# Performance work log

Hardware: AMD Instinct MI355X
Metric: run time of the kernel (lower is better)

Reference implementation:

```python
import jax, jax.numpy as jnp
import numpy as np

B = 4
T, Hh, Ww = 16, 32, 32
C = 256
HEADS = 8
WIN = 4
SHIFT = 2
MLP = 1024


def _rel_pos_index(w):
    coords = np.stack(np.meshgrid(np.arange(w), np.arange(w), np.arange(w), indexing='ij')).reshape(3, -1)
    rc = (coords[:, :, None] - coords[:, None, :]).transpose(1, 2, 0)
    rc[:, :, 0] += w - 1
    rc[:, :, 1] += w - 1
    rc[:, :, 2] += w - 1
    rc[:, :, 0] *= (2 * w - 1) * (2 * w - 1)
    rc[:, :, 1] *= 2 * w - 1
    return rc.sum(-1).astype(np.int32)  # (w^3, w^3)


def _attn_mask(t, h, w, win, shift):
    m = np.zeros((t, h, w))
    sl = (slice(0, -win), slice(-win, -shift), slice(-shift, None))
    cnt = 0
    for a in sl:
        for b in sl:
            for c in sl:
                m[a, b, c] = cnt
                cnt += 1
    m = m.reshape(t // win, win, h // win, win, w // win, win).transpose(0, 2, 4, 1, 3, 5).reshape(-1, win ** 3)
    am = m[:, None, :] - m[:, :, None]  # (nW, N, N)
    return np.where(am != 0, -100.0, 0.0).astype(np.float32)


def setup_inputs() -> dict:
    key = jax.random.key(0)
    ks = jax.random.split(key, 12)
    s_in = 1.0 / np.sqrt(C)
    s_mlp = 1.0 / np.sqrt(MLP)
    return {
        'x': jax.random.normal(ks[0], (B, T * Hh * Ww, C), jnp.float32),
        'norm1_g': jnp.ones((C,), jnp.float32),
        'norm1_b': jnp.zeros((C,), jnp.float32),
        'qkv_w': jax.random.normal(ks[1], (C, 3 * C), jnp.float32) * s_in,
        'qkv_b': jax.random.normal(ks[2], (3 * C,), jnp.float32) * 0.02,
        'proj_w': jax.random.normal(ks[3], (C, C), jnp.float32) * s_in,
        'proj_b': jax.random.normal(ks[4], (C,), jnp.float32) * 0.02,
        'rel_bias_table': jax.random.normal(ks[5], ((2 * WIN - 1) ** 3, HEADS), jnp.float32) * 0.02,
        'norm2_g': jnp.ones((C,), jnp.float32),
        'norm2_b': jnp.zeros((C,), jnp.float32),
        'mlp_w1': jax.random.normal(ks[6], (C, MLP), jnp.float32) * s_in,
        'mlp_b1': jax.random.normal(ks[7], (MLP,), jnp.float32) * 0.02,
        'mlp_w2': jax.random.normal(ks[8], (MLP, C), jnp.float32) * s_mlp,
        'mlp_b2': jax.random.normal(ks[9], (C,), jnp.float32) * 0.02,
        'rel_index': jnp.asarray(_rel_pos_index(WIN)),
        'attn_mask': jnp.asarray(_attn_mask(T, Hh, Ww, WIN, SHIFT)),
    }


def _ln(x, g, b, eps):
    mu = x.mean(-1, keepdims=True)
    var = ((x - mu) ** 2).mean(-1, keepdims=True)
    return (x - mu) * jax.lax.rsqrt(var + eps) * g + b


def reference(x, norm1_g, norm1_b, qkv_w, qkv_b, proj_w, proj_b, rel_bias_table,
              norm2_g, norm2_b, mlp_w1, mlp_b1, mlp_w2, mlp_b2, rel_index, attn_mask):
    w = WIN
    N = w ** 3
    hd = C // HEADS
    scale = hd ** -0.5

    h = _ln(x, norm1_g, norm1_b, 1e-5).reshape(B, T, Hh, Ww, C)
    h = jnp.roll(h, shift=(-SHIFT, -SHIFT, -SHIFT), axis=(1, 2, 3))
    # window partition -> (B*nW, N, C)
    h = h.reshape(B, T // w, w, Hh // w, w, Ww // w, w, C)
    h = h.transpose(0, 1, 3, 5, 2, 4, 6, 7).reshape(-1, N, C)

    qkv = (h @ qkv_w + qkv_b).reshape(-1, N, 3, HEADS, hd)
    qkv = qkv.transpose(2, 0, 3, 1, 4)  # (3, BW, heads, N, hd)
    q, k, v = qkv[0] * scale, qkv[1], qkv[2]
    attn = jnp.einsum('bhid,bhjd->bhij', q, k)

    bias = rel_bias_table[rel_index.reshape(-1)].reshape(N, N, HEADS).transpose(2, 0, 1)
    attn = attn + bias[None]

    nW = attn_mask.shape[0]
    attn = attn.reshape(-1, nW, HEADS, N, N) + attn_mask[None, :, None]
    attn = jax.nn.softmax(attn.reshape(-1, HEADS, N, N), axis=-1)

    o = jnp.einsum('bhij,bhjd->bhid', attn, v).transpose(0, 2, 1, 3).reshape(-1, N, C)
    o = o @ proj_w + proj_b
    # window reverse
    o = o.reshape(B, T // w, Hh // w, Ww // w, w, w, w, C)
    o = o.transpose(0, 1, 4, 2, 5, 3, 6, 7).reshape(B, T, Hh, Ww, C)
    o = jnp.roll(o, shift=(SHIFT, SHIFT, SHIFT), axis=(1, 2, 3)).reshape(B, T * Hh * Ww, C)

    x = x + o
    y = _ln(x, norm2_g, norm2_b, 1e-6)
    y = jax.nn.gelu(y @ mlp_w1 + mlp_b1, approximate=False) @ mlp_w2 + mlp_b2
    return x + y
```

## Files before the change

kernel.cpp:

```cpp
#include <hip/hip_runtime.h>
#include <cstdint>
#include <cstddef>

typedef float  f32x4_t  __attribute__((ext_vector_type(4)));
typedef __bf16 bf16x8_t __attribute__((ext_vector_type(8)));
typedef __bf16 bf16x4_t __attribute__((ext_vector_type(4)));

#define NTOK   65536
#define CCH    256
#define NWINT  1024

__device__ __forceinline__ float wred_sum(float v) {
#pragma unroll
  for (int off = 32; off > 0; off >>= 1) v += __shfl_xor(v, off, 64);
  return v;
}

__device__ __forceinline__ void gload16(void* lds, const void* g) {
  __builtin_amdgcn_global_load_lds(
      (const __attribute__((address_space(1))) uint32_t*)g,
      (__attribute__((address_space(3))) uint32_t*)lds, 16, 0, 0);
}

__device__ __forceinline__ int win_to_orig(int token) {
  int gid = token >> 6, n = token & 63;
  int bb = gid >> 8, rem = gid & 255;
  int t = (((rem >> 6) << 2) + (n >> 4) + 2) & 15;
  int h = ((((rem >> 3) & 7) << 2) + ((n >> 2) & 3) + 2) & 31;
  int w = (((rem & 7) << 2) + (n & 3) + 2) & 31;
  return ((bb * 16 + t) * 32 + h) * 32 + w;
}

__global__ __launch_bounds__(256) void prep_weights(
    const float* __restrict__ qkv_w, const float* __restrict__ proj_w,
    const float* __restrict__ mlp_w1, const float* __restrict__ mlp_w2,
    __bf16* __restrict__ wt_qkv, __bf16* __restrict__ wt_proj,
    __bf16* __restrict__ wt_mlp1, __bf16* __restrict__ wt_mlp2) {
  int i = blockIdx.x * 256 + threadIdx.x;
  if (i < 196608) {
    int k = i / 768, n = i % 768;
    wt_qkv[n * 256 + k] = (__bf16)qkv_w[i];
  } else if (i < 262144) {
    int j = i - 196608;
    int k = j >> 8, n = j & 255;
    wt_proj[n * 256 + k] = (__bf16)proj_w[j];
  } else if (i < 524288) {
    int j = i - 262144;
    int k = j >> 10, n = j & 1023;
    wt_mlp1[n * 256 + k] = (__bf16)mlp_w1[j];
  } else {
    int j = i - 524288;
    int k = j >> 8, n = j & 255;
    wt_mlp2[n * 1024 + k] = (__bf16)mlp_w2[j];
  }
}

__global__ __launch_bounds__(256) void cm_prep(
    const float* __restrict__ table, const int* __restrict__ ridx,
    const float* __restrict__ mask, __bf16* __restrict__ cm) {
  int tid = blockIdx.x * 256 + threadIdx.x;
  int l = tid & 63;
  int t16 = (tid >> 6) & 15;
  int h = (tid >> 10) & 7;
  int w = tid >> 13;
  int it = t16 & 3, jt = t16 >> 2;
  int i = it * 16 + (l & 15);
  int jb = jt * 16 + ((l >> 4) << 2);
  const float* mrow = mask + (size_t)w * 4096 + i * 64;
  const int* rrow = ridx + i * 64;
  bf16x4_t o;
#pragma unroll
  for (int r = 0; r < 4; ++r) {
    int j = jb + r;
    o[r] = (__bf16)(table[rrow[j] * 8 + h] + mrow[j]);
  }
  *(bf16x4_t*)(cm + (size_t)tid * 4) = o;
}

template <int MODE>
__global__ __launch_bounds__(256) void ln_kernel(
    const float* __restrict__ xin, const float* __restrict__ g,
    const float* __restrict__ b, __bf16* __restrict__ out, float eps) {
  int token = blockIdx.x * 4 + (threadIdx.x >> 6);
  int lane = threadIdx.x & 63;
  size_t src = (MODE == 0) ? (size_t)win_to_orig(token) : (size_t)token;
  f32x4_t v = ((const f32x4_t*)(xin + src * CCH))[lane];
  float mu = wred_sum(v[0] + v[1] + v[2] + v[3]) * (1.0f / 256.0f);
  float d0 = v[0] - mu, d1 = v[1] - mu, d2 = v[2] - mu, d3 = v[3] - mu;
  float var = wred_sum(d0 * d0 + d1 * d1 + d2 * d2 + d3 * d3) * (1.0f / 256.0f);
  float rs = rsqrtf(var + eps);
  f32x4_t gg = ((const f32x4_t*)g)[lane];
  f32x4_t bb = ((const f32x4_t*)b)[lane];
  bf16x4_t o;
  o[0] = (__bf16)(d0 * rs * gg[0] + bb[0]);
  o[1] = (__bf16)(d1 * rs * gg[1] + bb[1]);
  o[2] = (__bf16)(d2 * rs * gg[2] + bb[2]);
  o[3] = (__bf16)(d3 * rs * gg[3] + bb[3]);
  *(bf16x4_t*)(out + (size_t)token * CCH + lane * 4) = o;
}

#define BMG 128
#define BNG 256
#define BKG 64
template <int EPI>
__global__ __launch_bounds__(512, 4) void gemm_kernel(
    const __bf16* __restrict__ A, const __bf16* __restrict__ Bt,
    const float* __restrict__ bias, const float* __restrict__ res,
    void* __restrict__ outp, int M, int N, int K) {
  __shared__ __bf16 smA[BMG * BKG];
  __shared__ __bf16 smB[BNG * BKG];
  const int wv = threadIdx.x >> 6;
  const int ln = threadIdx.x & 63;
  const int i15 = ln & 15, g = ln >> 4;

  int nwg = gridDim.x;
  int wgid = ((int)blockIdx.x & 7) * (nwg >> 3) + ((int)blockIdx.x >> 3);
  int nx = N >> 8;
  int bx = wgid % nx, by = wgid / nx;
  const int bm = by * BMG, bn = bx * BNG;
  const int wr = wv >> 2, wc = wv & 3;

  const __bf16* aP[2];
  const __bf16* bP[4];
#pragma unroll
  for (int it = 0; it < 2; ++it) {
    int slot = (it * 8 + wv) * 64 + ln;
    int row = slot >> 3;
    int chunk = (slot & 7) ^ (row & 7);
    aP[it] = A + (size_t)(bm + row) * K + chunk * 8;
  }
#pragma unroll
  for (int it = 0; it < 4; ++it) {
    int slot = (it * 8 + wv) * 64 + ln;
    int row = slot >> 3;
    int chunk = (slot & 7) ^ (row & 7);
    bP[it] = Bt + (size_t)(bn + row) * K + chunk * 8;
  }

  f32x4_t acc[4][4];
#pragma unroll
  for (int m = 0; m < 4; ++m)
#pragma unroll
    for (int n = 0; n < 4; ++n) acc[m][n] = (f32x4_t){0.f, 0.f, 0.f, 0.f};

  const int KT = K >> 6;
  for (int kt = 0; kt < KT; ++kt) {
#pragma unroll
    for (int it = 0; it < 2; ++it) {
      gload16(&smA[(it * 8 + wv) * 512], aP[it]);
      aP[it] += BKG;
    }
#pragma unroll
    for (int it = 0; it < 4; ++it) {
      gload16(&smB[(it * 8 + wv) * 512], bP[it]);
      bP[it] += BKG;
    }
    asm volatile("s_waitcnt vmcnt(0)" ::: "memory");
    __syncthreads();

#pragma unroll
    for (int kh = 0; kh < 2; ++kh) {
      int co = ((kh * 4 + g) ^ (i15 & 7)) * 8;
      bf16x8_t af[4], bfr[4];
#pragma unroll
      for (int m = 0; m < 4; ++m)
        af[m] = *(const bf16x8_t*)(smA + (wr * 64 + m * 16 + i15) * 64 + co);
#pragma unroll
      for (int n = 0; n < 4; ++n)
        bfr[n] = *(const bf16x8_t*)(smB + (wc * 64 + n * 16 + i15) * 64 + co);
#pragma unroll
      for (int m = 0; m < 4; ++m)
#pragma unroll
        for (int n = 0; n < 4; ++n)
          acc[m][n] = __builtin_amdgcn_mfma_f32_16x16x32_bf16(
              af[m], bfr[n], acc[m][n], 0, 0, 0);
    }
    __syncthreads();
  }

  float bv[4];
#pragma unroll
  for (int n = 0; n < 4; ++n) bv[n] = bias[bn + wc * 64 + n * 16 + i15];
#pragma unroll
  for (int m = 0; m < 4; ++m) {
    int grow0 = bm + wr * 64 + m * 16 + g * 4;
#pragma unroll
    for (int r = 0; r < 4; ++r) {
      int grow = grow0 + r;
      size_t rowbase;
      if constexpr (EPI == 1)
        rowbase = (size_t)win_to_orig(grow) * CCH;
      else
        rowbase = (size_t)grow * N;
#pragma unroll
      for (int n = 0; n < 4; ++n) {
        int gcol = bn + wc * 64 + n * 16 + i15;
        float v = acc[m][n][r] + bv[n];
        if constexpr (EPI == 0) {
          ((__bf16*)outp)[rowbase + gcol] = (__bf16)v;
        } else if constexpr (EPI == 1) {
          size_t dst = rowbase + gcol;
          ((float*)outp)[dst] = res[dst] + v;
        } else if constexpr (EPI == 2) {
          float u = v * (0.7978845608028654f + 0.03567740814f * v * v);
          float t = 1.0f - 2.0f / (__expf(2.0f * u) + 1.0f);
          float gl = 0.5f * v * (1.0f + t);
          ((__bf16*)outp)[rowbase + gcol] = (__bf16)gl;
        } else {
          size_t o = rowbase + gcol;
          ((float*)outp)[o] = res[o] + v;
        }
      }
    }
  }
}

__global__ __launch_bounds__(256) void attn_mfma(
    const __bf16* __restrict__ qkv, const __bf16* __restrict__ cm,
    __bf16* __restrict__ owin) {
  __shared__ __align__(16) __bf16 smP[4][64 * 72];
  __shared__ __align__(16) __bf16 smV[4][64 * 32];
  const int wv = threadIdx.x >> 6;
  const int ln = threadIdx.x & 63;
  const int task = blockIdx.x * 4 + wv;
  const int win = task >> 3;
  const int h = task & 7;
  const int i15 = ln & 15, g = ln >> 4;

  const __bf16* base = qkv + (size_t)win * 64 * 768 + h * 32;

  {
    __bf16* vdst = smV[wv];
#pragma unroll
    for (int c = 0; c < 4; ++c) {
      const __bf16* src =
          base + (size_t)(c * 16 + (ln >> 2)) * 768 + 512 + (ln & 3) * 8;
      gload16(vdst + c * 512, src);
    }
  }

  bf16x8_t kf[4], qf[4];
#pragma unroll
  for (int t = 0; t < 4; ++t) {
    kf[t] = *(const bf16x8_t*)(base + (size_t)(t * 16 + i15) * 768 + 256 + g * 8);
    qf[t] = *(const bf16x8_t*)(base + (size_t)(t * 16 + i15) * 768 + g * 8);
  }

  f32x4_t st[4][4];
#pragma unroll
  for (int jt = 0; jt < 4; ++jt)
#pragma unroll
    for (int it = 0; it < 4; ++it)
      st[jt][it] = __builtin_amdgcn_mfma_f32_16x16x32_bf16(
          kf[jt], qf[it], (f32x4_t){0.f, 0.f, 0.f, 0.f}, 0, 0, 0);

  const __bf16* cmp = cm + (((size_t)(win & 255) * 8 + h) * 16) * 256;
#pragma unroll
  for (int jt = 0; jt < 4; ++jt)
#pragma unroll
    for (int it = 0; it < 4; ++it) {
      bf16x4_t c4 = *(const bf16x4_t*)(cmp + ((jt * 4 + it) * 64 + ln) * 4);
#pragma unroll
      for (int r = 0; r < 4; ++r)
        st[jt][it][r] =
            fmaf(st[jt][it][r], 0.17677669529663687f, (float)c4[r]);
    }

#pragma unroll
  for (int it = 0; it < 4; ++it) {
    float mx = -1e30f;
#pragma unroll
    for (int jt = 0; jt < 4; ++jt)
#pragma unroll
      for (int r = 0; r < 4; ++r) mx = fmaxf(mx, st[jt][it][r]);
    mx = fmaxf(mx, __shfl_xor(mx, 16, 64));
    mx = fmaxf(mx, __shfl_xor(mx, 32, 64));
    float sum = 0.f;
#pragma unroll
    for (int jt = 0; jt < 4; ++jt)
#pragma unroll
      for (int r = 0; r < 4; ++r) {
        float p = __expf(st[jt][it][r] - mx);
        st[jt][it][r] = p;
        sum += p;
      }
    sum += __shfl_xor(sum, 16, 64);
    sum += __shfl_xor(sum, 32, 64);
    float inv = 1.0f / sum;
#pragma unroll
    for (int jt = 0; jt < 4; ++jt) {
      bf16x4_t p4;
#pragma unroll
      for (int r = 0; r < 4; ++r) p4[r] = (__bf16)(st[jt][it][r] * inv);
      *(bf16x4_t*)(smP[wv] + (it * 16 + i15) * 72 + jt * 16 + g * 4) = p4;
    }
  }
  __syncthreads();

  f32x4_t oacc[4][2];
#pragma unroll
  for (int it = 0; it < 4; ++it)
#pragma unroll
    for (int dt = 0; dt < 2; ++dt) oacc[it][dt] = (f32x4_t){0.f, 0.f, 0.f, 0.f};

  const __bf16* pl = smP[wv];
  const __bf16* vl = smV[wv];
#pragma unroll
  for (int kt = 0; kt < 2; ++kt) {
    bf16x8_t vf[2];
#pragma unroll
    for (int dt = 0; dt < 2; ++dt)
#pragma unroll
      for (int e = 0; e < 8; ++e)
        vf[dt][e] = vl[(kt * 32 + g * 8 + e) * 32 + dt * 16 + i15];
#pragma unroll
    for (int it = 0; it < 4; ++it) {
      bf16x8_t pa =
          *(const bf16x8_t*)(pl + (it * 16 + i15) * 72 + kt * 32 + g * 8);
#pragma unroll
      for (int dt = 0; dt < 2; ++dt)
        oacc[it][dt] = __builtin_amdgcn_mfma_f32_16x16x32_bf16(
            pa, vf[dt], oacc[it][dt], 0, 0, 0);
    }
  }

  __bf16* op = owin + (size_t)win * 64 * 256 + h * 32;
#pragma unroll
  for (int it = 0; it < 4; ++it)
#pragma unroll
    for (int r = 0; r < 4; ++r) {
      int i = it * 16 + g * 4 + r;
#pragma unroll
      for (int dt = 0; dt < 2; ++dt)
        op[(size_t)i * 256 + dt * 16 + i15] = (__bf16)oacc[it][dt][r];
    }
}

extern "C" void kernel_launch(void* const* d_in, const int* in_sizes, int n_in,
                              void* d_out, int out_size, void* d_ws,
                              size_t ws_size, hipStream_t stream) {
  (void)in_sizes; (void)n_in; (void)out_size; (void)ws_size;
  const float* x      = (const float*)d_in[0];
  const float* n1g    = (const float*)d_in[1];
  const float* n1b    = (const float*)d_in[2];
  const float* qkv_w  = (const float*)d_in[3];
  const float* qkv_b  = (const float*)d_in[4];
  const float* proj_w = (const float*)d_in[5];
  const float* proj_b = (const float*)d_in[6];
  const float* rbt    = (const float*)d_in[7];
  const float* n2g    = (const float*)d_in[8];
  const float* n2b    = (const float*)d_in[9];
  const float* mlp_w1 = (const float*)d_in[10];
  const float* mlp_b1 = (const float*)d_in[11];
  const float* mlp_w2 = (const float*)d_in[12];
  const float* mlp_b2 = (const float*)d_in[13];
  const int*   ridx   = (const int*)d_in[14];
  const float* amask  = (const float*)d_in[15];

  char* ws = (char*)d_ws;
  size_t off = 0;
  auto alloc = [&](size_t bytes) {
    void* p = ws + off;
    off += (bytes + 255) & ~(size_t)255;
    return p;
  };
  __bf16* wt_qkv  = (__bf16*)alloc(768 * 256 * 2);
  __bf16* wt_proj = (__bf16*)alloc(256 * 256 * 2);
  __bf16* wt_mlp1 = (__bf16*)alloc(1024 * 256 * 2);
  __bf16* wt_mlp2 = (__bf16*)alloc(1024 * 256 * 2);
  __bf16* hwin = (__bf16*)alloc((size_t)NTOK * 256 * 2);
  __bf16* qkv  = (__bf16*)alloc((size_t)NTOK * 768 * 2);
  __bf16* owin = (__bf16*)alloc((size_t)NTOK * 256 * 2);
  __bf16* cmb  = hwin;
  __bf16* yb   = hwin;
  __bf16* mlph = qkv;
  float* x2    = (float*)d_out;

  prep_weights<<<3072, 256, 0, stream>>>(qkv_w, proj_w, mlp_w1, mlp_w2,
                                         wt_qkv, wt_proj, wt_mlp1, wt_mlp2);
  ln_kernel<0><<<NTOK / 4, 256, 0, stream>>>(x, n1g, n1b, hwin, 1e-5f);
  gemm_kernel<0><<<(768 / BNG) * (NTOK / BMG), 512, 0, stream>>>(
      hwin, wt_qkv, qkv_b, nullptr, qkv, NTOK, 768, 256);
  cm_prep<<<8192, 256, 0, stream>>>(rbt, ridx, amask, cmb);
  attn_mfma<<<2048, 256, 0, stream>>>(qkv, cmb, owin);
  gemm_kernel<1><<<(256 / BNG) * (NTOK / BMG), 512, 0, stream>>>(
      owin, wt_proj, proj_b, x, x2, NTOK, 256, 256);
  ln_kernel<1><<<NTOK / 4, 256, 0, stream>>>(x2, n2g, n2b, yb, 1e-6f);
  gemm_kernel<2><<<(1024 / BNG) * (NTOK / BMG), 512, 0, stream>>>(
      yb, wt_mlp1, mlp_b1, nullptr, mlph, NTOK, 1024, 256);
  gemm_kernel<3><<<(256 / BNG) * (NTOK / BMG), 512, 0, stream>>>(
      mlph, wt_mlp2, mlp_b2, x2, d_out, NTOK, 256, 1024);
}
```

Baseline: 303.6 us.

## Fuse projection with LayerNorm2 and fuse both MLP GEMMs with on-chip GELU

Projection GEMM now adds bias and residual, computes the second LayerNorm across waves through shared memory, and writes both x2 and the normalized bf16 activations in original token order. That removes the separate LN pass. The two MLP GEMMs are fused so the 1024-wide GELU hidden state stays in LDS chunk by chunk, which avoids the large bf16 intermediate round trip through global memory. The GEMM epilogues were transposed to vectorized stores. The trade-off is larger LDS footprints, lower occupancy (launch bounds 2), and more serialized weight loads per block.

```diff
diff --git a/kernel.cpp b/kernel.cpp
--- a/kernel.cpp
+++ b/kernel.cpp
@@ -29,6 +29,12 @@
   int h = ((((rem >> 3) & 7) << 2) + ((n >> 2) & 3) + 2) & 31;
   int w = (((rem & 7) << 2) + (n & 3) + 2) & 31;
   return ((bb * 16 + t) * 32 + h) * 32 + w;
+}
+
+__device__ __forceinline__ float gelu_f(float v) {
+  float u = v * (0.7978845608028654f + 0.03567740814f * v * v);
+  float t = 1.0f - 2.0f / (__expf(2.0f * u) + 1.0f);
+  return 0.5f * v * (1.0f + t);
 }
 
 __global__ __launch_bounds__(256) void prep_weights(
@@ -77,13 +83,12 @@
   *(bf16x4_t*)(cm + (size_t)tid * 4) = o;
 }
 
-template <int MODE>
 __global__ __launch_bounds__(256) void ln_kernel(
     const float* __restrict__ xin, const float* __restrict__ g,
     const float* __restrict__ b, __bf16* __restrict__ out, float eps) {
   int token = blockIdx.x * 4 + (threadIdx.x >> 6);
   int lane = threadIdx.x & 63;
-  size_t src = (MODE == 0) ? (size_t)win_to_orig(token) : (size_t)token;
+  size_t src = (size_t)win_to_orig(token);
   f32x4_t v = ((const f32x4_t*)(xin + src * CCH))[lane];
   float mu = wred_sum(v[0] + v[1] + v[2] + v[3]) * (1.0f / 256.0f);
   float d0 = v[0] - mu, d1 = v[1] - mu, d2 = v[2] - mu, d3 = v[3] - mu;
@@ -102,11 +107,10 @@
 #define BMG 128
 #define BNG 256
 #define BKG 64
-template <int EPI>
-__global__ __launch_bounds__(512, 4) void gemm_kernel(
+__global__ __launch_bounds__(512, 4) void gemm_qkv(
     const __bf16* __restrict__ A, const __bf16* __restrict__ Bt,
-    const float* __restrict__ bias, const float* __restrict__ res,
-    void* __restrict__ outp, int M, int N, int K) {
+    const float* __restrict__ bias, __bf16* __restrict__ outp,
+    int N, int K) {
   __shared__ __bf16 smA[BMG * BKG];
   __shared__ __bf16 smB[BNG * BKG];
   const int wv = threadIdx.x >> 6;
@@ -125,23 +129,21 @@
 #pragma unroll
   for (int it = 0; it < 2; ++it) {
     int slot = (it * 8 + wv) * 64 + ln;
-    int row = slot >> 3;
-    int chunk = (slot & 7) ^ (row & 7);
+    int row = slot >> 3, chunk = (slot & 7) ^ (row & 7);
     aP[it] = A + (size_t)(bm + row) * K + chunk * 8;
   }
 #pragma unroll
   for (int it = 0; it < 4; ++it) {
     int slot = (it * 8 + wv) * 64 + ln;
-    int row = slot >> 3;
-    int chunk = (slot & 7) ^ (row & 7);
+    int row = slot >> 3, chunk = (slot & 7) ^ (row & 7);
     bP[it] = Bt + (size_t)(bn + row) * K + chunk * 8;
   }
 
   f32x4_t acc[4][4];
 #pragma unroll
-  for (int m = 0; m < 4; ++m)
-#pragma unroll
-    for (int n = 0; n < 4; ++n) acc[m][n] = (f32x4_t){0.f, 0.f, 0.f, 0.f};
+  for (int nn = 0; nn < 4; ++nn)
+#pragma unroll
+    for (int mm = 0; mm < 4; ++mm) acc[nn][mm] = (f32x4_t){0.f, 0.f, 0.f, 0.f};
 
   const int KT = K >> 6;
   for (int kt = 0; kt < KT; ++kt) {
@@ -160,57 +162,327 @@
 
 #pragma unroll
     for (int kh = 0; kh < 2; ++kh) {
-      int co = ((kh * 4 + g) ^ (i15 & 7)) * 8;
+      int co = ((kh * 4 + g) ^ (i15 & 7)) * 16;
       bf16x8_t af[4], bfr[4];
 #pragma unroll
-      for (int m = 0; m < 4; ++m)
-        af[m] = *(const bf16x8_t*)(smA + (wr * 64 + m * 16 + i15) * 64 + co);
-#pragma unroll
-      for (int n = 0; n < 4; ++n)
-        bfr[n] = *(const bf16x8_t*)(smB + (wc * 64 + n * 16 + i15) * 64 + co);
-#pragma unroll
-      for (int m = 0; m < 4; ++m)
-#pragma unroll
-        for (int n = 0; n < 4; ++n)
-          acc[m][n] = __builtin_amdgcn_mfma_f32_16x16x32_bf16(
-              af[m], bfr[n], acc[m][n], 0, 0, 0);
+      for (int mm = 0; mm < 4; ++mm)
+        af[mm] = *(const bf16x8_t*)((const char*)smA +
+                                    (wr * 64 + mm * 16 + i15) * 128 + co);
+#pragma unroll
+      for (int nn = 0; nn < 4; ++nn)
+        bfr[nn] = *(const bf16x8_t*)((const char*)smB +
+                                     (wc * 64 + nn * 16 + i15) * 128 + co);
+#pragma unroll
+      for (int nn = 0; nn < 4; ++nn)
+#pragma unroll
+        for (int mm = 0; mm < 4; ++mm)
+          acc[nn][mm] = __builtin_amdgcn_mfma_f32_16x16x32_bf16(
+              bfr[nn], af[mm], acc[nn][mm], 0, 0, 0);
     }
     __syncthreads();
   }
 
-  float bv[4];
-#pragma unroll
-  for (int n = 0; n < 4; ++n) bv[n] = bias[bn + wc * 64 + n * 16 + i15];
-#pragma unroll
-  for (int m = 0; m < 4; ++m) {
-    int grow0 = bm + wr * 64 + m * 16 + g * 4;
-#pragma unroll
-    for (int r = 0; r < 4; ++r) {
-      int grow = grow0 + r;
-      size_t rowbase;
-      if constexpr (EPI == 1)
-        rowbase = (size_t)win_to_orig(grow) * CCH;
-      else
-        rowbase = (size_t)grow * N;
-#pragma unroll
-      for (int n = 0; n < 4; ++n) {
-        int gcol = bn + wc * 64 + n * 16 + i15;
-        float v = acc[m][n][r] + bv[n];
-        if constexpr (EPI == 0) {
-          ((__bf16*)outp)[rowbase + gcol] = (__bf16)v;
-        } else if constexpr (EPI == 1) {
-          size_t dst = rowbase + gcol;
-          ((float*)outp)[dst] = res[dst] + v;
-        } else if constexpr (EPI == 2) {
-          float u = v * (0.7978845608028654f + 0.03567740814f * v * v);
-          float t = 1.0f - 2.0f / (__expf(2.0f * u) + 1.0f);
-          float gl = 0.5f * v * (1.0f + t);
-          ((__bf16*)outp)[rowbase + gcol] = (__bf16)gl;
-        } else {
-          size_t o = rowbase + gcol;
-          ((float*)outp)[o] = res[o] + v;
-        }
+#pragma unroll
+  for (int nn = 0; nn < 4; ++nn) {
+    int colg = bn + wc * 64 + nn * 16 + g * 4;
+    f32x4_t bv = *(const f32x4_t*)(bias + colg);
+#pragma unroll
+    for (int mm = 0; mm < 4; ++mm) {
+      int rowg = bm + wr * 64 + mm * 16 + i15;
+      bf16x4_t o;
+#pragma unroll
+      for (int r = 0; r < 4; ++r) o[r] = (__bf16)(acc[nn][mm][r] + bv[r]);
+      *(bf16x4_t*)(outp + (size_t)rowg * N + colg) = o;
+    }
+  }
+}
+
+__global__ __launch_bounds__(512, 2) void proj_ln(
+    const __bf16* __restrict__ A, const __bf16* __restrict__ Bt,
+    const float* __restrict__ bias, const float* __restrict__ res,
+    const float* __restrict__ g2, const float* __restrict__ b2,
+    float* __restrict__ x2, __bf16* __restrict__ yb) {
+  __shared__ __bf16 smA[BMG * BKG];
+  __shared__ __bf16 smB[BNG * BKG];
+  const int wv = threadIdx.x >> 6;
+  const int ln = threadIdx.x & 63;
+  const int i15 = ln & 15, g = ln >> 4;
+
+  int nwg = gridDim.x;
+  int wgid = ((int)blockIdx.x & 7) * (nwg >> 3) + ((int)blockIdx.x >> 3);
+  const int bm = wgid * BMG;
+  const int wr = wv >> 2, wc = wv & 3;
+  const int K = 256;
+
+  const __bf16* aP[2];
+  const __bf16* bP[4];
+#pragma unroll
+  for (int it = 0; it < 2; ++it) {
+    int slot = (it * 8 + wv) * 64 + ln;
+    int row = slot >> 3, chunk = (slot & 7) ^ (row & 7);
+    aP[it] = A + (size_t)(bm + row) * K + chunk * 8;
+  }
+#pragma unroll
+  for (int it = 0; it < 4; ++it) {
+    int slot = (it * 8 + wv) * 64 + ln;
+    int row = slot >> 3, chunk = (slot & 7) ^ (row & 7);
+    bP[it] = Bt + (size_t)row * K + chunk * 8;
+  }
+
+  f32x4_t acc[4][4];
+#pragma unroll
+  for (int nn = 0; nn < 4; ++nn)
+#pragma unroll
+    for (int mm = 0; mm < 4; ++mm) acc[nn][mm] = (f32x4_t){0.f, 0.f, 0.f, 0.f};
+
+  for (int kt = 0; kt < 4; ++kt) {
+#pragma unroll
+    for (int it = 0; it < 2; ++it) {
+      gload16(&smA[(it * 8 + wv) * 512], aP[it]);
+      aP[it] += BKG;
+    }
+#pragma unroll
+    for (int it = 0; it < 4; ++it) {
+      gload16(&smB[(it * 8 + wv) * 512], bP[it]);
+      bP[it] += BKG;
+    }
+    asm volatile("s_waitcnt vmcnt(0)" ::: "memory");
+    __syncthreads();
+#pragma unroll
+    for (int kh = 0; kh < 2; ++kh) {
+      int co = ((kh * 4 + g) ^ (i15 & 7)) * 16;
+      bf16x8_t af[4], bfr[4];
+#pragma unroll
+      for (int mm = 0; mm < 4; ++mm)
+        af[mm] = *(const bf16x8_t*)((const char*)smA +
+                                    (wr * 64 + mm * 16 + i15) * 128 + co);
+#pragma unroll
+      for (int nn = 0; nn < 4; ++nn)
+        bfr[nn] = *(const bf16x8_t*)((const char*)smB +
+                                     (wc * 64 + nn * 16 + i15) * 128 + co);
+#pragma unroll
+      for (int nn = 0; nn < 4; ++nn)
+#pragma unroll
+        for (int mm = 0; mm < 4; ++mm)
+          acc[nn][mm] = __builtin_amdgcn_mfma_f32_16x16x32_bf16(
+              bfr[nn], af[mm], acc[nn][mm], 0, 0, 0);
+    }
+    __syncthreads();
+  }
+
+  size_t dst[4];
+#pragma unroll
+  for (int mm = 0; mm < 4; ++mm) {
+    int rowg = bm + wr * 64 + mm * 16 + i15;
+    dst[mm] = (size_t)win_to_orig(rowg) * CCH;
+  }
+#pragma unroll
+  for (int nn = 0; nn < 4; ++nn) {
+    int colg = wc * 64 + nn * 16 + g * 4;
+    f32x4_t bv = *(const f32x4_t*)(bias + colg);
+#pragma unroll
+    for (int mm = 0; mm < 4; ++mm) {
+      f32x4_t rv = *(const f32x4_t*)(res + dst[mm] + colg);
+#pragma unroll
+      for (int r = 0; r < 4; ++r) acc[nn][mm][r] += bv[r] + rv[r];
+    }
+  }
+
+  float2* stf = (float2*)smA;
+#pragma unroll
+  for (int mm = 0; mm < 4; ++mm) {
+    float s1 = 0.f, s2 = 0.f;
+#pragma unroll
+    for (int nn = 0; nn < 4; ++nn)
+#pragma unroll
+      for (int r = 0; r < 4; ++r) {
+        float v = acc[nn][mm][r];
+        s1 += v;
+        s2 += v * v;
       }
+    s1 += __shfl_xor(s1, 16, 64);
+    s1 += __shfl_xor(s1, 32, 64);
+    s2 += __shfl_xor(s2, 16, 64);
+    s2 += __shfl_xor(s2, 32, 64);
+    if (g == 0) stf[(wr * 64 + mm * 16 + i15) * 4 + wc] = make_float2(s1, s2);
+  }
+  __syncthreads();
+  float mu[4], rs[4];
+#pragma unroll
+  for (int mm = 0; mm < 4; ++mm) {
+    int row = wr * 64 + mm * 16 + i15;
+    float S1 = 0.f, S2 = 0.f;
+#pragma unroll
+    for (int w = 0; w < 4; ++w) {
+      float2 p = stf[row * 4 + w];
+      S1 += p.x;
+      S2 += p.y;
+    }
+    mu[mm] = S1 * (1.0f / 256.0f);
+    rs[mm] = rsqrtf(S2 * (1.0f / 256.0f) - mu[mm] * mu[mm] + 1e-6f);
+  }
+
+#pragma unroll
+  for (int nn = 0; nn < 4; ++nn) {
+    int colg = wc * 64 + nn * 16 + g * 4;
+    f32x4_t gv = *(const f32x4_t*)(g2 + colg);
+    f32x4_t bv = *(const f32x4_t*)(b2 + colg);
+#pragma unroll
+    for (int mm = 0; mm < 4; ++mm) {
+      f32x4_t v = acc[nn][mm];
+      *(f32x4_t*)(x2 + dst[mm] + colg) = v;
+      bf16x4_t yo;
+#pragma unroll
+      for (int r = 0; r < 4; ++r)
+        yo[r] = (__bf16)((v[r] - mu[mm]) * rs[mm] * gv[r] + bv[r]);
+      *(bf16x4_t*)(yb + dst[mm] + colg) = yo;
+    }
+  }
+}
+
+__global__ __launch_bounds__(256, 2) void mlp_fused(
+    const __bf16* __restrict__ yb, const __bf16* __restrict__ w1t,
+    const float* __restrict__ b1, const __bf16* __restrict__ w2t,
+    const float* __restrict__ b2, float* __restrict__ io) {
+  __shared__ __bf16 smA[64 * 64];
+  __shared__ __bf16 smW[256 * 64];
+  __shared__ __bf16 h1b[64 * 256];
+  const int wv = threadIdx.x >> 6;
+  const int ln = threadIdx.x & 63;
+  const int i15 = ln & 15, g = ln >> 4, wc = wv;
+
+  int nwg = gridDim.x;
+  int wgid = ((int)blockIdx.x & 7) * (nwg >> 3) + ((int)blockIdx.x >> 3);
+  const int bm = wgid * 64;
+
+  uint32_t aOff[2], w1o[8], w2o[8];
+#pragma unroll
+  for (int rnd = 0; rnd < 2; ++rnd) {
+    int slot = rnd * 256 + (int)threadIdx.x;
+    int row = slot >> 3, ch = (slot & 7) ^ (row & 7);
+    aOff[rnd] = (uint32_t)((bm + row) * 256 + ch * 8);
+  }
+#pragma unroll
+  for (int rnd = 0; rnd < 8; ++rnd) {
+    int slot = rnd * 256 + (int)threadIdx.x;
+    int row = slot >> 3, ch = (slot & 7) ^ (row & 7);
+    w1o[rnd] = (uint32_t)(row * 256 + ch * 8);
+    w2o[rnd] = (uint32_t)(row * 1024 + ch * 8);
+  }
+
+  f32x4_t acc2[4][4];
+#pragma unroll
+  for (int nn = 0; nn < 4; ++nn)
+#pragma unroll
+    for (int mm = 0; mm < 4; ++mm) acc2[nn][mm] = (f32x4_t){0.f, 0.f, 0.f, 0.f};
+
+  for (int nc = 0; nc < 4; ++nc) {
+    f32x4_t acc1[4][4];
+#pragma unroll
+    for (int nn = 0; nn < 4; ++nn)
+#pragma unroll
+      for (int mm = 0; mm < 4; ++mm)
+        acc1[nn][mm] = (f32x4_t){0.f, 0.f, 0.f, 0.f};
+
+    for (int kt = 0; kt < 4; ++kt) {
+#pragma unroll
+      for (int rnd = 0; rnd < 2; ++rnd)
+        gload16(&smA[(rnd * 4 + wv) * 512], yb + aOff[rnd] + kt * 64);
+#pragma unroll
+      for (int rnd = 0; rnd < 8; ++rnd)
+        gload16(&smW[(rnd * 4 + wv) * 512],
+                w1t + nc * 65536 + w1o[rnd] + kt * 64);
+      asm volatile("s_waitcnt vmcnt(0)" ::: "memory");
+      __syncthreads();
+#pragma unroll
+      for (int kh = 0; kh < 2; ++kh) {
+        int co = ((kh * 4 + g) ^ (i15 & 7)) * 16;
+        bf16x8_t af[4], wf[4];
+#pragma unroll
+        for (int mm = 0; mm < 4; ++mm)
+          af[mm] = *(const bf16x8_t*)((const char*)smA +
+                                      (mm * 16 + i15) * 128 + co);
+#pragma unroll
+        for (int nn = 0; nn < 4; ++nn)
+          wf[nn] = *(const bf16x8_t*)((const char*)smW +
+                                      (wc * 64 + nn * 16 + i15) * 128 + co);
+#pragma unroll
+        for (int nn = 0; nn < 4; ++nn)
+#pragma unroll
+          for (int mm = 0; mm < 4; ++mm)
+            acc1[nn][mm] = __builtin_amdgcn_mfma_f32_16x16x32_bf16(
+                wf[nn], af[mm], acc1[nn][mm], 0, 0, 0);
+      }
+      __syncthreads();
+    }
+
+#pragma unroll
+    for (int rnd = 0; rnd < 8; ++rnd)
+      gload16(&smW[(rnd * 4 + wv) * 512], w2t + w2o[rnd] + nc * 256);
+
+    const float* b1g = b1 + nc * 256 + wc * 64;
+#pragma unroll
+    for (int nn = 0; nn < 4; ++nn) {
+      f32x4_t bb = *(const f32x4_t*)(b1g + nn * 16 + g * 4);
+#pragma unroll
+      for (int mm = 0; mm < 4; ++mm) {
+        bf16x4_t p;
+#pragma unroll
+        for (int r = 0; r < 4; ++r)
+          p[r] = (__bf16)gelu_f(acc1[nn][mm][r] + bb[r]);
+        uint32_t byte =
+            (uint32_t)((mm * 16 + i15) * 512 +
+                       ((wc * 128 + nn * 32 + g * 8) ^ ((i15 & 7) << 4)));
+        *(bf16x4_t*)((char*)h1b + byte) = p;
+      }
+    }
+
+    for (int kt2 = 0; kt2 < 4; ++kt2) {
+      asm volatile("s_waitcnt vmcnt(0)" ::: "memory");
+      __syncthreads();
+#pragma unroll
+      for (int kh = 0; kh < 2; ++kh) {
+        int coW = ((kh * 4 + g) ^ (i15 & 7)) * 16;
+        int coA = kt2 * 128 + ((kh * 64 + g * 16) ^ ((i15 & 7) << 4));
+        bf16x8_t af[4], wf[4];
+#pragma unroll
+        for (int mm = 0; mm < 4; ++mm)
+          af[mm] = *(const bf16x8_t*)((const char*)h1b +
+                                      (mm * 16 + i15) * 512 + coA);
+#pragma unroll
+        for (int nn = 0; nn < 4; ++nn)
+          wf[nn] = *(const bf16x8_t*)((const char*)smW +
+                                      (wc * 64 + nn * 16 + i15) * 128 + coW);
+#pragma unroll
+        for (int nn = 0; nn < 4; ++nn)
+#pragma unroll
+          for (int mm = 0; mm < 4; ++mm)
+            acc2[nn][mm] = __builtin_amdgcn_mfma_f32_16x16x32_bf16(
+                wf[nn], af[mm], acc2[nn][mm], 0, 0, 0);
+      }
+      __syncthreads();
+      if (kt2 < 3) {
+#pragma unroll
+        for (int rnd = 0; rnd < 8; ++rnd)
+          gload16(&smW[(rnd * 4 + wv) * 512],
+                  w2t + w2o[rnd] + nc * 256 + (kt2 + 1) * 64);
+      }
+    }
+  }
+
+#pragma unroll
+  for (int nn = 0; nn < 4; ++nn) {
+    int colg = wc * 64 + nn * 16 + g * 4;
+    f32x4_t bb = *(const f32x4_t*)(b2 + colg);
+#pragma unroll
+    for (int mm = 0; mm < 4; ++mm) {
+      int rowg = bm + mm * 16 + i15;
+      float* p = io + (size_t)rowg * 256 + colg;
+      f32x4_t rv = *(const f32x4_t*)p;
+      f32x4_t o;
+#pragma unroll
+      for (int r = 0; r < 4; ++r) o[r] = rv[r] + acc2[nn][mm][r] + bb[r];
+      *(f32x4_t*)p = o;
     }
   }
 }
@@ -373,21 +645,17 @@
   __bf16* owin = (__bf16*)alloc((size_t)NTOK * 256 * 2);
   __bf16* cmb  = hwin;
   __bf16* yb   = hwin;
-  __bf16* mlph = qkv;
   float* x2    = (float*)d_out;
 
   prep_weights<<<3072, 256, 0, stream>>>(qkv_w, proj_w, mlp_w1, mlp_w2,
                                          wt_qkv, wt_proj, wt_mlp1, wt_mlp2);
-  ln_kernel<0><<<NTOK / 4, 256, 0, stream>>>(x, n1g, n1b, hwin, 1e-5f);
-  gemm_kernel<0><<<(768 / BNG) * (NTOK / BMG), 512, 0, stream>>>(
-      hwin, wt_qkv, qkv_b, nullptr, qkv, NTOK, 768, 256);
+  ln_kernel<<<NTOK / 4, 256, 0, stream>>>(x, n1g, n1b, hwin, 1e-5f);
+  gemm_qkv<<<3 * (NTOK / BMG), 512, 0, stream>>>(hwin, wt_qkv, qkv_b, qkv,
+                                                 768, 256);
   cm_prep<<<8192, 256, 0, stream>>>(rbt, ridx, amask, cmb);
   attn_mfma<<<2048, 256, 0, stream>>>(qkv, cmb, owin);
-  gemm_kernel<1><<<(256 / BNG) * (NTOK / BMG), 512, 0, stream>>>(
-      owin, wt_proj, proj_b, x, x2, NTOK, 256, 256);
-  ln_kernel<1><<<NTOK / 4, 256, 0, stream>>>(x2, n2g, n2b, yb, 1e-6f);
-  gemm_kernel<2><<<(1024 / BNG) * (NTOK / BMG), 512, 0, stream>>>(
-      yb, wt_mlp1, mlp_b1, nullptr, mlph, NTOK, 1024, 256);
-  gemm_kernel<3><<<(256 / BNG) * (NTOK / BMG), 512, 0, stream>>>(
-      mlph, wt_mlp2, mlp_b2, x2, d_out, NTOK, 256, 1024);
-}
+  proj_ln<<<NTOK / BMG, 512, 0, stream>>>(owin, wt_proj, proj_b, x, n2g, n2b,
+                                          x2, yb);
+  mlp_fused<<<NTOK / 64, 256, 0, stream>>>(yb, wt_mlp1, mlp_b1, wt_mlp2,
+                                           mlp_b2, x2);
+}
```

After: 317.2 us. 4.5% more time.

## Fuse projection GEMM, residual add and second LayerNorm into one kernel

Applied to the files above, without the earlier changes.

Replaces the separate projection GEMM (with residual epilogue) and the LN2 kernel with a single kernel. Each 128-row block covers the full 256-column output, so per-row mean and variance can be reduced in registers and shared memory. The kernel then writes both x2 in fp32 and the normalized bf16 input for the MLP. This removes one kernel launch and the re-read of x2 (64 MB fp32) by the LN kernel. In exchange it uses a one-pass variance formula (E[x²]−mu²) and adds extra LDS and synchronisation in the epilogue.

```diff
diff --git a/kernel.cpp b/kernel.cpp
--- a/kernel.cpp
+++ b/kernel.cpp
@@ -8,7 +8,6 @@
 
 #define NTOK   65536
 #define CCH    256
-#define NWINT  1024
 
 __device__ __forceinline__ float wred_sum(float v) {
 #pragma unroll
@@ -29,6 +28,12 @@
   int h = ((((rem >> 3) & 7) << 2) + ((n >> 2) & 3) + 2) & 31;
   int w = (((rem & 7) << 2) + (n & 3) + 2) & 31;
   return ((bb * 16 + t) * 32 + h) * 32 + w;
+}
+
+__device__ __forceinline__ float gelu_f(float v) {
+  float u = v * (0.7978845608028654f + 0.03567740814f * v * v);
+  float t = 1.0f - 2.0f / (__expf(2.0f * u) + 1.0f);
+  return 0.5f * v * (1.0f + t);
 }
 
 __global__ __launch_bounds__(256) void prep_weights(
@@ -77,13 +82,12 @@
   *(bf16x4_t*)(cm + (size_t)tid * 4) = o;
 }
 
-template <int MODE>
 __global__ __launch_bounds__(256) void ln_kernel(
     const float* __restrict__ xin, const float* __restrict__ g,
     const float* __restrict__ b, __bf16* __restrict__ out, float eps) {
   int token = blockIdx.x * 4 + (threadIdx.x >> 6);
   int lane = threadIdx.x & 63;
-  size_t src = (MODE == 0) ? (size_t)win_to_orig(token) : (size_t)token;
+  size_t src = (size_t)win_to_orig(token);
   f32x4_t v = ((const f32x4_t*)(xin + src * CCH))[lane];
   float mu = wred_sum(v[0] + v[1] + v[2] + v[3]) * (1.0f / 256.0f);
   float d0 = v[0] - mu, d1 = v[1] - mu, d2 = v[2] - mu, d3 = v[3] - mu;
@@ -125,15 +129,13 @@
 #pragma unroll
   for (int it = 0; it < 2; ++it) {
     int slot = (it * 8 + wv) * 64 + ln;
-    int row = slot >> 3;
-    int chunk = (slot & 7) ^ (row & 7);
+    int row = slot >> 3, chunk = (slot & 7) ^ (row & 7);
     aP[it] = A + (size_t)(bm + row) * K + chunk * 8;
   }
 #pragma unroll
   for (int it = 0; it < 4; ++it) {
     int slot = (it * 8 + wv) * 64 + ln;
-    int row = slot >> 3;
-    int chunk = (slot & 7) ^ (row & 7);
+    int row = slot >> 3, chunk = (slot & 7) ^ (row & 7);
     bP[it] = Bt + (size_t)(bn + row) * K + chunk * 8;
   }
 
@@ -160,14 +162,16 @@
 
 #pragma unroll
     for (int kh = 0; kh < 2; ++kh) {
-      int co = ((kh * 4 + g) ^ (i15 & 7)) * 8;
+      int co = ((kh * 4 + g) ^ (i15 & 7)) * 16;
       bf16x8_t af[4], bfr[4];
 #pragma unroll
       for (int m = 0; m < 4; ++m)
-        af[m] = *(const bf16x8_t*)(smA + (wr * 64 + m * 16 + i15) * 64 + co);
+        af[m] = *(const bf16x8_t*)((const char*)smA +
+                                   (wr * 64 + m * 16 + i15) * 128 + co);
 #pragma unroll
       for (int n = 0; n < 4; ++n)
-        bfr[n] = *(const bf16x8_t*)(smB + (wc * 64 + n * 16 + i15) * 64 + co);
+        bfr[n] = *(const bf16x8_t*)((const char*)smB +
+                                    (wc * 64 + n * 16 + i15) * 128 + co);
 #pragma unroll
       for (int m = 0; m < 4; ++m)
 #pragma unroll
@@ -187,29 +191,170 @@
 #pragma unroll
     for (int r = 0; r < 4; ++r) {
       int grow = grow0 + r;
-      size_t rowbase;
-      if constexpr (EPI == 1)
-        rowbase = (size_t)win_to_orig(grow) * CCH;
-      else
-        rowbase = (size_t)grow * N;
+      size_t rowbase = (size_t)grow * N;
 #pragma unroll
       for (int n = 0; n < 4; ++n) {
         int gcol = bn + wc * 64 + n * 16 + i15;
         float v = acc[m][n][r] + bv[n];
         if constexpr (EPI == 0) {
           ((__bf16*)outp)[rowbase + gcol] = (__bf16)v;
-        } else if constexpr (EPI == 1) {
-          size_t dst = rowbase + gcol;
-          ((float*)outp)[dst] = res[dst] + v;
         } else if constexpr (EPI == 2) {
-          float u = v * (0.7978845608028654f + 0.03567740814f * v * v);
-          float t = 1.0f - 2.0f / (__expf(2.0f * u) + 1.0f);
-          float gl = 0.5f * v * (1.0f + t);
-          ((__bf16*)outp)[rowbase + gcol] = (__bf16)gl;
+          ((__bf16*)outp)[rowbase + gcol] = (__bf16)gelu_f(v);
         } else {
           size_t o = rowbase + gcol;
           ((float*)outp)[o] = res[o] + v;
         }
+      }
+    }
+  }
+}
+
+__global__ __launch_bounds__(512, 4) void proj_ln(
+    const __bf16* __restrict__ A, const __bf16* __restrict__ Bt,
+    const float* __restrict__ bias, const float* __restrict__ res,
+    const float* __restrict__ g2, const float* __restrict__ b2,
+    float* __restrict__ x2, __bf16* __restrict__ yb) {
+  constexpr int K = 256;
+  __shared__ __bf16 smA[BMG * BKG];
+  __shared__ __bf16 smB[BNG * BKG];
+  __shared__ float2 stf[512];
+  const int wv = threadIdx.x >> 6;
+  const int ln = threadIdx.x & 63;
+  const int i15 = ln & 15, g = ln >> 4;
+
+  int nwg = gridDim.x;
+  int wgid = ((int)blockIdx.x & 7) * (nwg >> 3) + ((int)blockIdx.x >> 3);
+  const int bm = wgid * BMG, bn = 0;
+  const int wr = wv >> 2, wc = wv & 3;
+
+  const __bf16* aP[2];
+  const __bf16* bP[4];
+#pragma unroll
+  for (int it = 0; it < 2; ++it) {
+    int slot = (it * 8 + wv) * 64 + ln;
+    int row = slot >> 3, chunk = (slot & 7) ^ (row & 7);
+    aP[it] = A + (size_t)(bm + row) * K + chunk * 8;
+  }
+#pragma unroll
+  for (int it = 0; it < 4; ++it) {
+    int slot = (it * 8 + wv) * 64 + ln;
+    int row = slot >> 3, chunk = (slot & 7) ^ (row & 7);
+    bP[it] = Bt + (size_t)(bn + row) * K + chunk * 8;
+  }
+
+  f32x4_t acc[4][4];
+#pragma unroll
+  for (int m = 0; m < 4; ++m)
+#pragma unroll
+    for (int n = 0; n < 4; ++n) acc[m][n] = (f32x4_t){0.f, 0.f, 0.f, 0.f};
+
+  for (int kt = 0; kt < 4; ++kt) {
+#pragma unroll
+    for (int it = 0; it < 2; ++it) {
+      gload16(&smA[(it * 8 + wv) * 512], aP[it]);
+      aP[it] += BKG;
+    }
+#pragma unroll
+    for (int it = 0; it < 4; ++it) {
+      gload16(&smB[(it * 8 + wv) * 512], bP[it]);
+      bP[it] += BKG;
+    }
+    asm volatile("s_waitcnt vmcnt(0)" ::: "memory");
+    __syncthreads();
+
+#pragma unroll
+    for (int kh = 0; kh < 2; ++kh) {
+      int co = ((kh * 4 + g) ^ (i15 & 7)) * 16;
+      bf16x8_t af[4], bfr[4];
+#pragma unroll
+      for (int m = 0; m < 4; ++m)
+        af[m] = *(const bf16x8_t*)((const char*)smA +
+                                   (wr * 64 + m * 16 + i15) * 128 + co);
+#pragma unroll
+      for (int n = 0; n < 4; ++n)
+        bfr[n] = *(const bf16x8_t*)((const char*)smB +
+                                    (wc * 64 + n * 16 + i15) * 128 + co);
+#pragma unroll
+      for (int m = 0; m < 4; ++m)
+#pragma unroll
+        for (int n = 0; n < 4; ++n)
+          acc[m][n] = __builtin_amdgcn_mfma_f32_16x16x32_bf16(
+              af[m], bfr[n], acc[m][n], 0, 0, 0);
+    }
+    __syncthreads();
+  }
+
+  float bv[4];
+#pragma unroll
+  for (int n = 0; n < 4; ++n) bv[n] = bias[wc * 64 + n * 16 + i15];
+#pragma unroll
+  for (int m = 0; m < 4; ++m) {
+    int grow0 = bm + wr * 64 + m * 16 + g * 4;
+#pragma unroll
+    for (int r = 0; r < 4; ++r) {
+      size_t rowbase = (size_t)win_to_orig(grow0 + r) * CCH;
+#pragma unroll
+      for (int n = 0; n < 4; ++n) {
+        int gcol = wc * 64 + n * 16 + i15;
+        acc[m][n][r] += bv[n] + res[rowbase + gcol];
+      }
+    }
+  }
+
+#pragma unroll
+  for (int m = 0; m < 4; ++m) {
+#pragma unroll
+    for (int r = 0; r < 4; ++r) {
+      float s1 = 0.f, s2 = 0.f;
+#pragma unroll
+      for (int n = 0; n < 4; ++n) {
+        float v = acc[m][n][r];
+        s1 += v;
+        s2 += v * v;
+      }
+      s1 += __shfl_xor(s1, 1, 64);
+      s1 += __shfl_xor(s1, 2, 64);
+      s1 += __shfl_xor(s1, 4, 64);
+      s1 += __shfl_xor(s1, 8, 64);
+      s2 += __shfl_xor(s2, 1, 64);
+      s2 += __shfl_xor(s2, 2, 64);
+      s2 += __shfl_xor(s2, 4, 64);
+      s2 += __shfl_xor(s2, 8, 64);
+      if (i15 == 0)
+        stf[(wr * 64 + m * 16 + g * 4 + r) * 4 + wc] = make_float2(s1, s2);
+    }
+  }
+  __syncthreads();
+
+  float gv[4], bv2[4];
+#pragma unroll
+  for (int n = 0; n < 4; ++n) {
+    int gcol = wc * 64 + n * 16 + i15;
+    gv[n] = g2[gcol];
+    bv2[n] = b2[gcol];
+  }
+#pragma unroll
+  for (int m = 0; m < 4; ++m) {
+    int grow0 = bm + wr * 64 + m * 16 + g * 4;
+#pragma unroll
+    for (int r = 0; r < 4; ++r) {
+      int row_local = wr * 64 + m * 16 + g * 4 + r;
+      float S1 = 0.f, S2 = 0.f;
+#pragma unroll
+      for (int w = 0; w < 4; ++w) {
+        float2 p = stf[row_local * 4 + w];
+        S1 += p.x;
+        S2 += p.y;
+      }
+      float mu = S1 * (1.0f / 256.0f);
+      float rsv = rsqrtf(S2 * (1.0f / 256.0f) - mu * mu + 1e-6f);
+      size_t rowbase = (size_t)win_to_orig(grow0 + r) * CCH;
+#pragma unroll
+      for (int n = 0; n < 4; ++n) {
+        int gcol = wc * 64 + n * 16 + i15;
+        float v = acc[m][n][r];
+        x2[rowbase + gcol] = v;
+        yb[rowbase + gcol] = (__bf16)((v - mu) * rsv * gv[n] + bv2[n]);
       }
     }
   }
@@ -378,14 +523,13 @@
 
   prep_weights<<<3072, 256, 0, stream>>>(qkv_w, proj_w, mlp_w1, mlp_w2,
                                          wt_qkv, wt_proj, wt_mlp1, wt_mlp2);
-  ln_kernel<0><<<NTOK / 4, 256, 0, stream>>>(x, n1g, n1b, hwin, 1e-5f);
+  ln_kernel<<<NTOK / 4, 256, 0, stream>>>(x, n1g, n1b, hwin, 1e-5f);
   gemm_kernel<0><<<(768 / BNG) * (NTOK / BMG), 512, 0, stream>>>(
       hwin, wt_qkv, qkv_b, nullptr, qkv, NTOK, 768, 256);
   cm_prep<<<8192, 256, 0, stream>>>(rbt, ridx, amask, cmb);
   attn_mfma<<<2048, 256, 0, stream>>>(qkv, cmb, owin);
-  gemm_kernel<1><<<(256 / BNG) * (NTOK / BMG), 512, 0, stream>>>(
-      owin, wt_proj, proj_b, x, x2, NTOK, 256, 256);
-  ln_kernel<1><<<NTOK / 4, 256, 0, stream>>>(x2, n2g, n2b, yb, 1e-6f);
+  proj_ln<<<NTOK / BMG, 512, 0, stream>>>(owin, wt_proj, proj_b, x, n2g, n2b,
+                                          x2, yb);
   gemm_kernel<2><<<(1024 / BNG) * (NTOK / BMG), 512, 0, stream>>>(
       yb, wt_mlp1, mlp_b1, nullptr, mlph, NTOK, 1024, 256);
   gemm_kernel<3><<<(256 / BNG) * (NTOK / BMG), 512, 0, stream>>>(
```

Measured after the change: 355.5 us. 17.1% more time.
